# Kernel tuning notes

Hardware: AMD Instinct MI355X
Metric: run time of the kernel (lower is better)

The kernel has to match this reference:

```python
import jax, jax.numpy as jnp
import numpy as np

B, C, H, W = 8, 128, 192, 192
CROP = 39
LEN = CROP // 2            # 19 -> 38x38 crop
CY = CX = 96               # fixed crop center (original draws random.randint(19, 173))
MARGIN = 1.0


def grid_sample_bilinear(img, grid):
    """Bilinear grid_sample, align_corners=True, zeros padding.
    img: (B,C,H,W); grid: (B,H,W,2) with (x,y) in [-1,1]."""
    _, _, Hi, Wi = img.shape
    gx = (grid[..., 0] + 1.0) * 0.5 * (Wi - 1)   # (B,H,W) source x
    gy = (grid[..., 1] + 1.0) * 0.5 * (Hi - 1)   # (B,H,W) source y
    x0 = jnp.floor(gx)
    y0 = jnp.floor(gy)

    def gather(xf, yf):
        valid = (xf >= 0) & (xf <= Wi - 1) & (yf >= 0) & (yf <= Hi - 1)
        xi = jnp.clip(xf, 0, Wi - 1).astype(jnp.int32)
        yi = jnp.clip(yf, 0, Hi - 1).astype(jnp.int32)
        # per-batch gather: (C,H,W) values at integer (y,x) locations
        v = jax.vmap(lambda im, y, x: im[:, y, x])(img, yi, xi)  # (B,C,H,W)
        return v * valid[:, None, :, :].astype(img.dtype)

    wx1 = gx - x0
    wx0 = 1.0 - wx1
    wy1 = gy - y0
    wy0 = 1.0 - wy1
    w = lambda a: a[:, None, :, :]
    return (w(wx0 * wy0) * gather(x0,       y0)
          + w(wx1 * wy0) * gather(x0 + 1.0, y0)
          + w(wx0 * wy1) * gather(x0,       y0 + 1.0)
          + w(wx1 * wy1) * gather(x0 + 1.0, y0 + 1.0))


def hardnet_loss(anchor, positive, margin=MARGIN):
    """loss_HardNet with anchor_swap=False, batch_reduce='min', triplet_margin."""
    d1 = jnp.sum(anchor * anchor, axis=1)                       # (N,)
    d2 = jnp.sum(positive * positive, axis=1)                   # (N,)
    sq = d1[:, None] + d2[None, :] - 2.0 * (anchor @ positive.T)  # (N,N)
    dm = jnp.sqrt(jnp.maximum(sq, 0.0) + 1e-6) + 1e-8
    n = dm.shape[0]
    pos = jnp.diagonal(dm)                                      # positive distances
    dmod = dm + jnp.eye(n, dtype=dm.dtype) * 10.0               # mask diagonal
    dmod = dmod + jnp.where(dmod < 0.008, 10.0, 0.0)            # mask near-duplicates
    min_neg = jnp.min(dmod, axis=1)                             # hardest negative per anchor
    return jnp.mean(jnp.maximum(margin + pos - min_neg, 0.0))


def setup_inputs() -> dict:
    key = jax.random.key(0)
    k1, k2, k3 = jax.random.split(key, 3)
    feat1 = jax.random.normal(k1, (B, C, H, W), dtype=jnp.float32)
    feat2 = jax.random.normal(k2, (B, C, H, W), dtype=jnp.float32)
    # absolute flow: pixel coordinates in [0, W-1] / [0, H-1]
    aflow = jax.random.uniform(k3, (B, 2, H, W), dtype=jnp.float32) * (W - 1)
    return {"feat1": feat1, "feat2": feat2, "aflow": aflow}


def reference(feat1, feat2, aflow):
    # _aflow_to_grid: pixel coords -> [-1,1] grid (align_corners=True convention)
    gx = aflow[:, 0] * (2.0 / (W - 1)) - 1.0
    gy = aflow[:, 1] * (2.0 / (H - 1)) - 1.0
    grid = jnp.stack([gx, gy], axis=-1)                          # (B,H,W,2)
    grid = jnp.where(jnp.isnan(grid), 9e9, grid)                 # invalid -> out of range
    feat2to1 = grid_sample_bilinear(feat2, grid)                 # warp img2 feats to img1
    s = slice(CY - LEN, CY + LEN)                                # fixed 38x38 crop
    f1 = feat1[:, :, s, s]
    f2 = feat2to1[:, :, s, s]
    a = f1.transpose(0, 2, 3, 1).reshape(-1, C)                  # (B*38*38, C)
    p = f2.transpose(0, 2, 3, 1).reshape(-1, C)
    return hardnet_loss(a, p)
```

## Files before the change

kernel.cpp:

```cpp
#include <hip/hip_runtime.h>
#include <stdint.h>

#define Hh 192
#define Ww 192
#define HW 36864
#define CROPW 38
#define CW2 1444
#define CROPOFF 77
#define NPTS 11552
#define NPAD 11776
#define NTT 46
#define NCT 92
#define NG 5
#define JPB 19
#define NBLK (NG*NTT)
#define BIGF 3.0e38f

typedef short bf16x8 __attribute__((ext_vector_type(8)));
typedef float f32x4 __attribute__((ext_vector_type(4)));
typedef int   i32x4 __attribute__((ext_vector_type(4)));
typedef unsigned short ushort;

__device__ __forceinline__ ushort f2bf(float f) {
  uint32_t b = __float_as_uint(f);
  uint32_t r = b + 0x7fffu + ((b >> 16) & 1u);
  return (ushort)(r >> 16);
}
__device__ __forceinline__ float bf2f(ushort u) {
  return __uint_as_float(((uint32_t)u) << 16);
}

__device__ __forceinline__ void g2l16(const void* g, void* l) {
  __builtin_amdgcn_global_load_lds(
      (const __attribute__((address_space(1))) unsigned int*)g,
      (__attribute__((address_space(3))) unsigned int*)l, 16, 0, 0);
}

__global__ void init_k(ushort* __restrict__ aB, ushort* __restrict__ pB,
                       float* __restrict__ d1, float* __restrict__ d2) {
  int i = NPTS + threadIdx.x;
  if (i >= NPAD) return;
  d1[i] = 0.f;
  d2[i] = 1e30f;
  i32x4 z = {0,0,0,0};
  #pragma unroll
  for (int c = 0; c < 16; ++c) {
    *(i32x4*)&aB[(size_t)i*128 + c*8] = z;
    *(i32x4*)&pB[(size_t)i*128 + c*8] = z;
  }
}

__global__ __launch_bounds__(256) void transpose_k(
    const float* __restrict__ feat2, ushort* __restrict__ f2t) {
  __shared__ __align__(16) ushort l[32*136];
  int b = blockIdx.y;
  int hw0 = blockIdx.x * 32;
  int t = threadIdx.x;
  {
    int i4 = (t & 7) * 4, c0 = t >> 3;
    const float* src = feat2 + (size_t)b*128*HW + hw0 + i4;
    #pragma unroll
    for (int k = 0; k < 4; ++k) {
      int cc = c0 + k*32;
      f32x4 v = *(const f32x4*)(src + (size_t)cc*HW);
      #pragma unroll
      for (int j = 0; j < 4; ++j) l[(i4+j)*136 + cc] = f2bf(v[j]);
    }
  }
  __syncthreads();
  {
    int chunk = t & 7, p = t >> 3;
    ushort* dst = f2t + ((size_t)b*HW + hw0 + p)*128 + chunk*16;
    *(bf16x8*)dst       = *(const bf16x8*)&l[p*136 + chunk*16];
    *(bf16x8*)(dst + 8) = *(const bf16x8*)&l[p*136 + chunk*16 + 8];
  }
}

__global__ __launch_bounds__(256) void crop_k(
    const float* __restrict__ feat1, ushort* __restrict__ aB,
    float* __restrict__ d1) {
  __shared__ __align__(16) ushort l[38*136];
  int r = blockIdx.x;
  int b = blockIdx.y;
  int y = CROPOFF + r;
  int t = threadIdx.x;
  {
    int xo = t & 63, c0 = t >> 6;
    if (xo < CROPW) {
      const float* src = feat1 + ((size_t)b*128*HW) + (size_t)y*Ww + CROPOFF + xo;
      #pragma unroll
      for (int k = 0; k < 32; ++k) {
        int cc = c0*32 + k;
        l[xo*136 + cc] = f2bf(src[(size_t)cc*HW]);
      }
    }
  }
  __syncthreads();
  int chunk = t & 7, p0 = t >> 3;
  #pragma unroll
  for (int pp = 0; pp < 2; ++pp) {
    int p = p0 + pp*32;
    if (p >= CROPW) break;
    int idx = b*CW2 + r*CROPW + p;
    ushort* dst = aB + (size_t)idx*128 + chunk*16;
    *(bf16x8*)dst       = *(const bf16x8*)&l[p*136 + chunk*16];
    *(bf16x8*)(dst + 8) = *(const bf16x8*)&l[p*136 + chunk*16 + 8];
    float s = 0.f;
    #pragma unroll
    for (int j = 0; j < 16; ++j) {
      float v = bf2f(l[p*136 + chunk*16 + j]);
      s += v*v;
    }
    s += __shfl_xor(s, 1); s += __shfl_xor(s, 2); s += __shfl_xor(s, 4);
    if (chunk == 0) d1[idx] = s;
  }
}

__global__ __launch_bounds__(256) void samp2_k(
    const ushort* __restrict__ f2t, const float* __restrict__ aflow,
    ushort* __restrict__ pB, float* __restrict__ d2) {
  int tid = threadIdx.x;
  int idx = blockIdx.x*2 + (tid >> 7);
  int c = tid & 127;
  int b = idx / CW2;
  int rem = idx % CW2;
  int r = rem / CROPW, cx = rem % CROPW;
  int y = CROPOFF + r, x = CROPOFF + cx;

  float ax = aflow[((b*2 + 0)*Hh + y)*Ww + x];
  float ay = aflow[((b*2 + 1)*Hh + y)*Ww + x];
  float gxn = ax * (2.0f/(Ww-1)) - 1.0f;
  float gyn = ay * (2.0f/(Hh-1)) - 1.0f;
  float gx = (gxn + 1.0f) * 0.5f * (Ww-1);
  float gy = (gyn + 1.0f) * 0.5f * (Hh-1);
  int xi = min((int)floorf(gx), Ww-2);
  int yi = min((int)floorf(gy), Hh-2);
  float wx1 = gx - (float)xi, wx0 = 1.f - wx1;
  float wy1 = gy - (float)yi, wy0 = 1.f - wy1;

  const ushort* base = f2t + ((size_t)b*HW + (size_t)yi*Ww + xi)*128 + c;
  float v00 = bf2f(base[0]);
  float v01 = bf2f(base[128]);
  float v10 = bf2f(base[Ww*128]);
  float v11 = bf2f(base[Ww*128 + 128]);
  float v = wy0*(wx0*v00 + wx1*v01) + wy1*(wx0*v10 + wx1*v11);

  pB[(size_t)idx*128 + c] = f2bf(v);

  float s = v*v;
  for (int off = 1; off < 64; off <<= 1) s += __shfl_xor(s, off);
  __shared__ float red[4];
  if ((tid & 63) == 0) red[tid >> 6] = s;
  __syncthreads();
  if ((tid & 127) == 0) {
    int g = tid >> 7;
    d2[idx] = red[2*g] + red[2*g + 1];
  }
}

__global__ __launch_bounds__(512) void gemmp_k(
    const ushort* __restrict__ aB, const ushort* __restrict__ pB,
    const float* __restrict__ d1, const float* __restrict__ d2,
    float* __restrict__ pos, float* __restrict__ pmin) {
  __shared__ __align__(16) ushort lA[256*128];
  __shared__ __align__(16) ushort lB[2][128*128];

  int bid = blockIdx.x;
  int xcd = bid & 7, k = bid >> 3;
  int start = (xcd < 6) ? xcd*29 : 174 + (xcd-6)*28;
  int L = start + k;
  int g = L / NTT, tM = L % NTT;
  int j0 = g * JPB;
  int jn = (NCT - j0 < JPB) ? (NCT - j0) : JPB;

  int tid = threadIdx.x;
  int rowg = tid >> 4, cb = (tid & 15) << 4;

  {
    const char* gA = (const char*)aB + (size_t)tM * 65536;
    #pragma unroll
    for (int rnd = 0; rnd < 8; ++rnd) {
      int row = rnd*32 + rowg;
      g2l16(gA + row*256 + (cb ^ ((row&7)<<4)), (char*)lA + row*256 + cb);
    }
  }
  {
    const char* gB = (const char*)pB + (size_t)j0 * 128 * 256;
    #pragma unroll
    for (int rnd = 0; rnd < 4; ++rnd) {
      int row = rnd*32 + rowg;
      g2l16(gB + row*256 + (cb ^ ((row&7)<<4)), (char*)lB[0] + row*256 + cb);
    }
  }
  __syncthreads();

  int w = tid >> 6, l = tid & 63;
  int wr = w >> 1, wc = w & 1;
  int lcol = l & 15, hq = l >> 4, rb = hq << 2;
  int rsw = (lcol & 7) << 4;
  float mPart[4] = {BIGF, BIGF, BIGF, BIGF};

  for (int it = 0; it < jn; ++it) {
    int j = j0 + it;
    if (it + 1 < jn) {
      const char* gB = (const char*)pB + (size_t)(j+1) * 128 * 256;
      char* dst = (char*)lB[(it+1) & 1];
      #pragma unroll
      for (int rnd = 0; rnd < 4; ++rnd) {
        int row = rnd*32 + rowg;
        g2l16(gB + row*256 + (cb ^ ((row&7)<<4)), dst + row*256 + cb);
      }
    }
    const char* bufB = (const char*)lB[it & 1];
    f32x4 acc[4][4] = {};
    #pragma unroll
    for (int ks = 0; ks < 4; ++ks) {
      int cbase = ks*64 + (hq << 4);
      bf16x8 aF[4], bF[4];
      #pragma unroll
      for (int ma = 0; ma < 4; ++ma)
        aF[ma] = *(const bf16x8*)((const char*)lA + (wr*64 + ma*16 + lcol)*256 + (cbase ^ rsw));
      #pragma unroll
      for (int np = 0; np < 4; ++np)
        bF[np] = *(const bf16x8*)(bufB + (wc*64 + np*16 + lcol)*256 + (cbase ^ rsw));
      #pragma unroll
      for (int np = 0; np < 4; ++np)
        #pragma unroll
        for (int ma = 0; ma < 4; ++ma)
          acc[np][ma] = __builtin_amdgcn_mfma_f32_16x16x32_bf16(bF[np], aF[ma], acc[np][ma], 0, 0, 0);
    }

    f32x4 d2v[4];
    #pragma unroll
    for (int np = 0; np < 4; ++np)
      d2v[np] = *(const f32x4*)&d2[j*128 + wc*64 + np*16 + rb];

    if ((j >> 1) != tM) {
      #pragma unroll
      for (int ma = 0; ma < 4; ++ma)
        #pragma unroll
        for (int np = 0; np < 4; ++np)
          #pragma unroll
          for (int reg = 0; reg < 4; ++reg)
            mPart[ma] = fminf(mPart[ma], fmaf(-2.f, acc[np][ma][reg], d2v[np][reg]));
    } else {
      #pragma unroll
      for (int ma = 0; ma < 4; ++ma) {
        int gi = tM*256 + wr*64 + ma*16 + lcol;
        #pragma unroll
        for (int np = 0; np < 4; ++np)
          #pragma unroll
          for (int reg = 0; reg < 4; ++reg) {
            int gj = j*128 + wc*64 + np*16 + rb + reg;
            float t = fmaf(-2.f, acc[np][ma][reg], d2v[np][reg]);
            if (gi == gj)
              pos[gi] = sqrtf(fmaxf(d1[gi] + t, 0.f) + 1e-6f) + 1e-8f;
            else
              mPart[ma] = fminf(mPart[ma], t);
          }
      }
    }
    __syncthreads();
  }

  #pragma unroll
  for (int ma = 0; ma < 4; ++ma) {
    float u = mPart[ma];
    u = fminf(u, __shfl_xor(u, 16));
    u = fminf(u, __shfl_xor(u, 32));
    mPart[ma] = u;
  }
  __syncthreads();
  float* sm = (float*)lB;
  if (hq == 0) {
    #pragma unroll
    for (int ma = 0; ma < 4; ++ma)
      sm[wc*256 + wr*64 + ma*16 + lcol] = mPart[ma];
  }
  __syncthreads();
  if (tid < 256) {
    int row = tM*256 + tid;
    float u = fminf(sm[tid], sm[256 + tid]);
    float dm = sqrtf(fmaxf(d1[row] + u, 0.f) + 1e-6f) + 1e-8f;
    pmin[g*NPAD + row] = dm;
  }
}

__global__ __launch_bounds__(1024) void fin_k(const float* __restrict__ pos,
                                              const float* __restrict__ pmin,
                                              float* __restrict__ out) {
  float s = 0.f;
  for (int i = threadIdx.x; i < NPTS; i += 1024) {
    float p = pos[i];
    float mneg = p + 10.f;
    #pragma unroll
    for (int g = 0; g < NG; ++g) mneg = fminf(mneg, pmin[g*NPAD + i]);
    s += fmaxf(1.0f + p - mneg, 0.f);
  }
  for (int off = 1; off < 64; off <<= 1) s += __shfl_xor(s, off);
  __shared__ float red[16];
  if ((threadIdx.x & 63) == 0) red[threadIdx.x >> 6] = s;
  __syncthreads();
  if (threadIdx.x == 0) {
    float t = 0.f;
    #pragma unroll
    for (int k = 0; k < 16; ++k) t += red[k];
    out[0] = t / (float)NPTS;
  }
}

extern "C" void kernel_launch(void* const* d_in, const int* in_sizes, int n_in,
                              void* d_out, int out_size, void* d_ws, size_t ws_size,
                              hipStream_t stream) {
  const float* feat1 = (const float*)d_in[0];
  const float* feat2 = (const float*)d_in[1];
  const float* aflow = (const float*)d_in[2];

  char* ws = (char*)d_ws;
  ushort* aB = (ushort*)ws;
  ushort* pB = aB + (size_t)NPAD * 128;
  float*  d1 = (float*)(pB + (size_t)NPAD * 128);
  float*  d2 = d1 + NPAD;
  float*  pos = d2 + NPAD;
  float*  pmin = pos + NPAD;
  ushort* f2t = (ushort*)(pmin + (size_t)NG*NPAD);

  hipLaunchKernelGGL(transpose_k, dim3(HW/32, 8), dim3(256), 0, stream,
                     feat2, f2t);
  hipLaunchKernelGGL(init_k, dim3(1), dim3(256), 0, stream,
                     aB, pB, d1, d2);
  hipLaunchKernelGGL(crop_k, dim3(CROPW, 8), dim3(256), 0, stream,
                     feat1, aB, d1);
  hipLaunchKernelGGL(samp2_k, dim3(NPTS/2), dim3(256), 0, stream,
                     f2t, aflow, pB, d2);
  hipLaunchKernelGGL(gemmp_k, dim3(NBLK), dim3(512), 0, stream,
                     aB, pB, d1, d2, pos, pmin);
  hipLaunchKernelGGL(fin_k, dim3(1), dim3(1024), 0, stream,
                     pos, pmin, (float*)d_out);
}
```

Measured before the change: 107.2 us.

## Hold GEMM A tile in registers, stream B from global, fuse prep kernels

The distance GEMM no longer stages tiles in LDS. Each wave keeps a 128-row slice of the anchor tile in registers and reads positive fragments straight from global memory, which removes the LDS copies and per-iteration barriers; the kernel is now bounded to two blocks per CU. The feat2 transpose and feat1 crop are merged into one launch, and the padding initialisation moves into an extra block of the sampler, which cuts two launches. The sampler now handles two channels per lane, with one wave per point and a wave shuffle reduction in place of the LDS reduction. The trade-offs are much higher register pressure and redundant global and L2 traffic for B, and the padding rows of aB and d1 are no longer zeroed.

Measured after the change: 116.6 us. +8.7%, slower.

```diff
diff --git a/kernel.cpp b/kernel.cpp
--- a/kernel.cpp
+++ b/kernel.cpp
@@ -14,6 +14,7 @@
 #define NG 5
 #define JPB 19
 #define NBLK (NG*NTT)
+#define TRB (HW/32)
 #define BIGF 3.0e38f
 
 typedef short bf16x8 __attribute__((ext_vector_type(8)));
@@ -30,89 +31,65 @@
   return __uint_as_float(((uint32_t)u) << 16);
 }
 
-__device__ __forceinline__ void g2l16(const void* g, void* l) {
-  __builtin_amdgcn_global_load_lds(
-      (const __attribute__((address_space(1))) unsigned int*)g,
-      (__attribute__((address_space(3))) unsigned int*)l, 16, 0, 0);
-}
-
-__global__ void init_k(ushort* __restrict__ aB, ushort* __restrict__ pB,
-                       float* __restrict__ d1, float* __restrict__ d2) {
-  int i = NPTS + threadIdx.x;
-  if (i >= NPAD) return;
-  d1[i] = 0.f;
-  d2[i] = 1e30f;
-  i32x4 z = {0,0,0,0};
-  #pragma unroll
-  for (int c = 0; c < 16; ++c) {
-    *(i32x4*)&aB[(size_t)i*128 + c*8] = z;
-    *(i32x4*)&pB[(size_t)i*128 + c*8] = z;
-  }
-}
-
-__global__ __launch_bounds__(256) void transpose_k(
-    const float* __restrict__ feat2, ushort* __restrict__ f2t) {
-  __shared__ __align__(16) ushort l[32*136];
+__global__ __launch_bounds__(256) void prep_k(
+    const float* __restrict__ feat1, const float* __restrict__ feat2,
+    ushort* __restrict__ f2t, ushort* __restrict__ aB, float* __restrict__ d1) {
+  __shared__ __align__(16) ushort lsh[38*136];
   int b = blockIdx.y;
-  int hw0 = blockIdx.x * 32;
   int t = threadIdx.x;
-  {
-    int i4 = (t & 7) * 4, c0 = t >> 3;
-    const float* src = feat2 + (size_t)b*128*HW + hw0 + i4;
-    #pragma unroll
-    for (int k = 0; k < 4; ++k) {
-      int cc = c0 + k*32;
-      f32x4 v = *(const f32x4*)(src + (size_t)cc*HW);
-      #pragma unroll
-      for (int j = 0; j < 4; ++j) l[(i4+j)*136 + cc] = f2bf(v[j]);
-    }
-  }
-  __syncthreads();
-  {
-    int chunk = t & 7, p = t >> 3;
-    ushort* dst = f2t + ((size_t)b*HW + hw0 + p)*128 + chunk*16;
-    *(bf16x8*)dst       = *(const bf16x8*)&l[p*136 + chunk*16];
-    *(bf16x8*)(dst + 8) = *(const bf16x8*)&l[p*136 + chunk*16 + 8];
-  }
-}
-
-__global__ __launch_bounds__(256) void crop_k(
-    const float* __restrict__ feat1, ushort* __restrict__ aB,
-    float* __restrict__ d1) {
-  __shared__ __align__(16) ushort l[38*136];
-  int r = blockIdx.x;
-  int b = blockIdx.y;
-  int y = CROPOFF + r;
-  int t = threadIdx.x;
-  {
-    int xo = t & 63, c0 = t >> 6;
-    if (xo < CROPW) {
-      const float* src = feat1 + ((size_t)b*128*HW) + (size_t)y*Ww + CROPOFF + xo;
-      #pragma unroll
-      for (int k = 0; k < 32; ++k) {
-        int cc = c0*32 + k;
-        l[xo*136 + cc] = f2bf(src[(size_t)cc*HW]);
-      }
-    }
-  }
-  __syncthreads();
-  int chunk = t & 7, p0 = t >> 3;
-  #pragma unroll
-  for (int pp = 0; pp < 2; ++pp) {
-    int p = p0 + pp*32;
-    if (p >= CROPW) break;
-    int idx = b*CW2 + r*CROPW + p;
-    ushort* dst = aB + (size_t)idx*128 + chunk*16;
-    *(bf16x8*)dst       = *(const bf16x8*)&l[p*136 + chunk*16];
-    *(bf16x8*)(dst + 8) = *(const bf16x8*)&l[p*136 + chunk*16 + 8];
-    float s = 0.f;
-    #pragma unroll
-    for (int j = 0; j < 16; ++j) {
-      float v = bf2f(l[p*136 + chunk*16 + j]);
-      s += v*v;
-    }
-    s += __shfl_xor(s, 1); s += __shfl_xor(s, 2); s += __shfl_xor(s, 4);
-    if (chunk == 0) d1[idx] = s;
+  if (blockIdx.x < TRB) {
+    int hw0 = blockIdx.x * 32;
+    {
+      int i4 = (t & 7) * 4, c0 = t >> 3;
+      const float* src = feat2 + (size_t)b*128*HW + hw0 + i4;
+      #pragma unroll
+      for (int k = 0; k < 4; ++k) {
+        int cc = c0 + k*32;
+        f32x4 v = *(const f32x4*)(src + (size_t)cc*HW);
+        #pragma unroll
+        for (int j = 0; j < 4; ++j) lsh[(i4+j)*136 + cc] = f2bf(v[j]);
+      }
+    }
+    __syncthreads();
+    {
+      int chunk = t & 7, p = t >> 3;
+      ushort* dst = f2t + ((size_t)b*HW + hw0 + p)*128 + chunk*16;
+      *(bf16x8*)dst       = *(const bf16x8*)&lsh[p*136 + chunk*16];
+      *(bf16x8*)(dst + 8) = *(const bf16x8*)&lsh[p*136 + chunk*16 + 8];
+    }
+  } else {
+    int r = blockIdx.x - TRB;
+    int y = CROPOFF + r;
+    {
+      int xo = t & 63, c0 = t >> 6;
+      if (xo < CROPW) {
+        const float* src = feat1 + ((size_t)b*128*HW) + (size_t)y*Ww + CROPOFF + xo;
+        #pragma unroll
+        for (int k = 0; k < 32; ++k) {
+          int cc = c0*32 + k;
+          lsh[xo*136 + cc] = f2bf(src[(size_t)cc*HW]);
+        }
+      }
+    }
+    __syncthreads();
+    int chunk = t & 7, p0 = t >> 3;
+    #pragma unroll
+    for (int pp = 0; pp < 2; ++pp) {
+      int p = p0 + pp*32;
+      if (p >= CROPW) break;
+      int idx = b*CW2 + r*CROPW + p;
+      ushort* dst = aB + (size_t)idx*128 + chunk*16;
+      *(bf16x8*)dst       = *(const bf16x8*)&lsh[p*136 + chunk*16];
+      *(bf16x8*)(dst + 8) = *(const bf16x8*)&lsh[p*136 + chunk*16 + 8];
+      float s = 0.f;
+      #pragma unroll
+      for (int j = 0; j < 16; ++j) {
+        float v = bf2f(lsh[p*136 + chunk*16 + j]);
+        s += v*v;
+      }
+      s += __shfl_xor(s, 1); s += __shfl_xor(s, 2); s += __shfl_xor(s, 4);
+      if (chunk == 0) d1[idx] = s;
+    }
   }
 }
 
@@ -120,8 +97,18 @@
     const ushort* __restrict__ f2t, const float* __restrict__ aflow,
     ushort* __restrict__ pB, float* __restrict__ d2) {
   int tid = threadIdx.x;
-  int idx = blockIdx.x*2 + (tid >> 7);
-  int c = tid & 127;
+  if (blockIdx.x == NPTS/4) {
+    int i = NPTS + tid;
+    if (i < NPAD) {
+      d2[i] = 1e30f;
+      i32x4 z = {0,0,0,0};
+      #pragma unroll
+      for (int c = 0; c < 16; ++c) *(i32x4*)&pB[(size_t)i*128 + c*8] = z;
+    }
+    return;
+  }
+  int idx = blockIdx.x*4 + (tid >> 6);
+  int l = tid & 63, c2 = l*2;
   int b = idx / CW2;
   int rem = idx % CW2;
   int r = rem / CROPW, cx = rem % CROPW;
@@ -138,151 +125,120 @@
   float wx1 = gx - (float)xi, wx0 = 1.f - wx1;
   float wy1 = gy - (float)yi, wy0 = 1.f - wy1;
 
-  const ushort* base = f2t + ((size_t)b*HW + (size_t)yi*Ww + xi)*128 + c;
-  float v00 = bf2f(base[0]);
-  float v01 = bf2f(base[128]);
-  float v10 = bf2f(base[Ww*128]);
-  float v11 = bf2f(base[Ww*128 + 128]);
-  float v = wy0*(wx0*v00 + wx1*v01) + wy1*(wx0*v10 + wx1*v11);
-
-  pB[(size_t)idx*128 + c] = f2bf(v);
-
-  float s = v*v;
+  const ushort* base = f2t + ((size_t)b*HW + (size_t)yi*Ww + xi)*128 + c2;
+  uint32_t u00 = *(const uint32_t*)(base);
+  uint32_t u01 = *(const uint32_t*)(base + 128);
+  uint32_t u10 = *(const uint32_t*)(base + Ww*128);
+  uint32_t u11 = *(const uint32_t*)(base + Ww*128 + 128);
+  float v0 = wy0*(wx0*bf2f((ushort)u00) + wx1*bf2f((ushort)u01))
+           + wy1*(wx0*bf2f((ushort)u10) + wx1*bf2f((ushort)u11));
+  float v1 = wy0*(wx0*bf2f((ushort)(u00>>16)) + wx1*bf2f((ushort)(u01>>16)))
+           + wy1*(wx0*bf2f((ushort)(u10>>16)) + wx1*bf2f((ushort)(u11>>16)));
+
+  uint32_t packed = ((uint32_t)f2bf(v1) << 16) | f2bf(v0);
+  *(uint32_t*)&pB[(size_t)idx*128 + c2] = packed;
+
+  float s = v0*v0 + v1*v1;
   for (int off = 1; off < 64; off <<= 1) s += __shfl_xor(s, off);
-  __shared__ float red[4];
-  if ((tid & 63) == 0) red[tid >> 6] = s;
-  __syncthreads();
-  if ((tid & 127) == 0) {
-    int g = tid >> 7;
-    d2[idx] = red[2*g] + red[2*g + 1];
-  }
-}
-
-__global__ __launch_bounds__(512) void gemmp_k(
+  if (l == 0) d2[idx] = s;
+}
+
+__global__ __launch_bounds__(512, 2) void gemmp_k(
     const ushort* __restrict__ aB, const ushort* __restrict__ pB,
     const float* __restrict__ d1, const float* __restrict__ d2,
     float* __restrict__ pos, float* __restrict__ pmin) {
-  __shared__ __align__(16) ushort lA[256*128];
-  __shared__ __align__(16) ushort lB[2][128*128];
+  __shared__ float sm[4][256];
 
   int bid = blockIdx.x;
-  int xcd = bid & 7, k = bid >> 3;
+  int xcd = bid & 7, kk = bid >> 3;
   int start = (xcd < 6) ? xcd*29 : 174 + (xcd-6)*28;
-  int L = start + k;
+  int L = start + kk;
   int g = L / NTT, tM = L % NTT;
   int j0 = g * JPB;
   int jn = (NCT - j0 < JPB) ? (NCT - j0) : JPB;
 
   int tid = threadIdx.x;
-  int rowg = tid >> 4, cb = (tid & 15) << 4;
-
+  int w = tid >> 6, l = tid & 63;
+  int wr = w >> 2, wc = w & 3;
+  int lcol = l & 15, hq = l >> 4, rb = hq << 2;
+
+  bf16x8 aF[32];
   {
-    const char* gA = (const char*)aB + (size_t)tM * 65536;
-    #pragma unroll
-    for (int rnd = 0; rnd < 8; ++rnd) {
-      int row = rnd*32 + rowg;
-      g2l16(gA + row*256 + (cb ^ ((row&7)<<4)), (char*)lA + row*256 + cb);
-    }
-  }
-  {
-    const char* gB = (const char*)pB + (size_t)j0 * 128 * 256;
-    #pragma unroll
-    for (int rnd = 0; rnd < 4; ++rnd) {
-      int row = rnd*32 + rowg;
-      g2l16(gB + row*256 + (cb ^ ((row&7)<<4)), (char*)lB[0] + row*256 + cb);
-    }
-  }
-  __syncthreads();
-
-  int w = tid >> 6, l = tid & 63;
-  int wr = w >> 1, wc = w & 1;
-  int lcol = l & 15, hq = l >> 4, rb = hq << 2;
-  int rsw = (lcol & 7) << 4;
-  float mPart[4] = {BIGF, BIGF, BIGF, BIGF};
+    const char* gA = (const char*)aB + ((size_t)(tM*256 + wr*128 + lcol))*256 + hq*16;
+    #pragma unroll
+    for (int ma = 0; ma < 8; ++ma)
+      #pragma unroll
+      for (int ks = 0; ks < 4; ++ks)
+        aF[ma*4+ks] = *(const bf16x8*)(gA + ma*16*256 + ks*64);
+  }
+
+  float mPart[8] = {BIGF,BIGF,BIGF,BIGF,BIGF,BIGF,BIGF,BIGF};
 
   for (int it = 0; it < jn; ++it) {
     int j = j0 + it;
-    if (it + 1 < jn) {
-      const char* gB = (const char*)pB + (size_t)(j+1) * 128 * 256;
-      char* dst = (char*)lB[(it+1) & 1];
-      #pragma unroll
-      for (int rnd = 0; rnd < 4; ++rnd) {
-        int row = rnd*32 + rowg;
-        g2l16(gB + row*256 + (cb ^ ((row&7)<<4)), dst + row*256 + cb);
-      }
-    }
-    const char* bufB = (const char*)lB[it & 1];
-    f32x4 acc[4][4] = {};
+    const char* gB = (const char*)pB + ((size_t)(j*128 + wc*32 + lcol))*256 + hq*16;
+    f32x4 acc[2][8] = {};
     #pragma unroll
     for (int ks = 0; ks < 4; ++ks) {
-      int cbase = ks*64 + (hq << 4);
-      bf16x8 aF[4], bF[4];
-      #pragma unroll
-      for (int ma = 0; ma < 4; ++ma)
-        aF[ma] = *(const bf16x8*)((const char*)lA + (wr*64 + ma*16 + lcol)*256 + (cbase ^ rsw));
-      #pragma unroll
-      for (int np = 0; np < 4; ++np)
-        bF[np] = *(const bf16x8*)(bufB + (wc*64 + np*16 + lcol)*256 + (cbase ^ rsw));
-      #pragma unroll
-      for (int np = 0; np < 4; ++np)
-        #pragma unroll
-        for (int ma = 0; ma < 4; ++ma)
-          acc[np][ma] = __builtin_amdgcn_mfma_f32_16x16x32_bf16(bF[np], aF[ma], acc[np][ma], 0, 0, 0);
-    }
-
-    f32x4 d2v[4];
-    #pragma unroll
-    for (int np = 0; np < 4; ++np)
-      d2v[np] = *(const f32x4*)&d2[j*128 + wc*64 + np*16 + rb];
+      bf16x8 b0 = *(const bf16x8*)(gB + ks*64);
+      bf16x8 b1 = *(const bf16x8*)(gB + 16*256 + ks*64);
+      #pragma unroll
+      for (int ma = 0; ma < 8; ++ma)
+        acc[0][ma] = __builtin_amdgcn_mfma_f32_16x16x32_bf16(b0, aF[ma*4+ks], acc[0][ma], 0, 0, 0);
+      #pragma unroll
+      for (int ma = 0; ma < 8; ++ma)
+        acc[1][ma] = __builtin_amdgcn_mfma_f32_16x16x32_bf16(b1, aF[ma*4+ks], acc[1][ma], 0, 0, 0);
+    }
+
+    f32x4 d2v0 = *(const f32x4*)&d2[j*128 + wc*32 + rb];
+    f32x4 d2v1 = *(const f32x4*)&d2[j*128 + wc*32 + 16 + rb];
 
     if ((j >> 1) != tM) {
       #pragma unroll
-      for (int ma = 0; ma < 4; ++ma)
-        #pragma unroll
-        for (int np = 0; np < 4; ++np)
-          #pragma unroll
-          for (int reg = 0; reg < 4; ++reg)
-            mPart[ma] = fminf(mPart[ma], fmaf(-2.f, acc[np][ma][reg], d2v[np][reg]));
+      for (int ma = 0; ma < 8; ++ma) {
+        #pragma unroll
+        for (int reg = 0; reg < 4; ++reg) {
+          mPart[ma] = fminf(mPart[ma], fmaf(-2.f, acc[0][ma][reg], d2v0[reg]));
+          mPart[ma] = fminf(mPart[ma], fmaf(-2.f, acc[1][ma][reg], d2v1[reg]));
+        }
+      }
     } else {
       #pragma unroll
-      for (int ma = 0; ma < 4; ++ma) {
-        int gi = tM*256 + wr*64 + ma*16 + lcol;
-        #pragma unroll
-        for (int np = 0; np < 4; ++np)
+      for (int ma = 0; ma < 8; ++ma) {
+        int gi = tM*256 + wr*128 + ma*16 + lcol;
+        #pragma unroll
+        for (int np = 0; np < 2; ++np) {
           #pragma unroll
           for (int reg = 0; reg < 4; ++reg) {
-            int gj = j*128 + wc*64 + np*16 + rb + reg;
-            float t = fmaf(-2.f, acc[np][ma][reg], d2v[np][reg]);
+            int gj = j*128 + wc*32 + np*16 + rb + reg;
+            float t = fmaf(-2.f, acc[np][ma][reg], np ? d2v1[reg] : d2v0[reg]);
             if (gi == gj)
               pos[gi] = sqrtf(fmaxf(d1[gi] + t, 0.f) + 1e-6f) + 1e-8f;
             else
               mPart[ma] = fminf(mPart[ma], t);
           }
-      }
-    }
-    __syncthreads();
+        }
+      }
+    }
   }
 
   #pragma unroll
-  for (int ma = 0; ma < 4; ++ma) {
+  for (int ma = 0; ma < 8; ++ma) {
     float u = mPart[ma];
     u = fminf(u, __shfl_xor(u, 16));
     u = fminf(u, __shfl_xor(u, 32));
     mPart[ma] = u;
   }
-  __syncthreads();
-  float* sm = (float*)lB;
   if (hq == 0) {
     #pragma unroll
-    for (int ma = 0; ma < 4; ++ma)
-      sm[wc*256 + wr*64 + ma*16 + lcol] = mPart[ma];
+    for (int ma = 0; ma < 8; ++ma)
+      sm[wc][wr*128 + ma*16 + lcol] = mPart[ma];
   }
   __syncthreads();
   if (tid < 256) {
     int row = tM*256 + tid;
-    float u = fminf(sm[tid], sm[256 + tid]);
-    float dm = sqrtf(fmaxf(d1[row] + u, 0.f) + 1e-6f) + 1e-8f;
-    pmin[g*NPAD + row] = dm;
+    float u = fminf(fminf(sm[0][tid], sm[1][tid]), fminf(sm[2][tid], sm[3][tid]));
+    pmin[g*NPAD + row] = sqrtf(fmaxf(d1[row] + u, 0.f) + 1e-6f) + 1e-8f;
   }
 }
 
@@ -325,13 +281,9 @@
   float*  pmin = pos + NPAD;
   ushort* f2t = (ushort*)(pmin + (size_t)NG*NPAD);
 
-  hipLaunchKernelGGL(transpose_k, dim3(HW/32, 8), dim3(256), 0, stream,
-                     feat2, f2t);
-  hipLaunchKernelGGL(init_k, dim3(1), dim3(256), 0, stream,
-                     aB, pB, d1, d2);
-  hipLaunchKernelGGL(crop_k, dim3(CROPW, 8), dim3(256), 0, stream,
-                     feat1, aB, d1);
-  hipLaunchKernelGGL(samp2_k, dim3(NPTS/2), dim3(256), 0, stream,
+  hipLaunchKernelGGL(prep_k, dim3(TRB + CROPW, 8), dim3(256), 0, stream,
+                     feat1, feat2, f2t, aB, d1);
+  hipLaunchKernelGGL(samp2_k, dim3(NPTS/4 + 1), dim3(256), 0, stream,
                      f2t, aflow, pB, d2);
   hipLaunchKernelGGL(gemmp_k, dim3(NBLK), dim3(512), 0, stream,
                      aB, pB, d1, d2, pos, pmin);
```

## Sample warped features from per-channel LDS planes instead of transposed copy

Applied to the files above, without the earlier changes.

Removes the full feat2 transpose into a bf16 channel-last buffer. Each block now loads one (batch, channel) plane into LDS as bf16 and bilinearly samples all crop points from precomputed coordinates. Crop extraction and coordinate computation are merged into one launch, and the squared norms move to a separate pass that also zero-pads the tail rows. The GEMM keeps its A fragments in registers rather than staging them in LDS. This trades a large transposed write and re-read for 72KB LDS planes and scattered 2-byte stores into pB, plus higher register pressure in the GEMM.

Result: faster. 98.19 us (-8.4%).

```diff
diff --git a/kernel.cpp b/kernel.cpp
--- a/kernel.cpp
+++ b/kernel.cpp
@@ -14,11 +14,14 @@
 #define NG 5
 #define JPB 19
 #define NBLK (NG*NTT)
+#define CROPB 304
+#define CRDB 46
 #define BIGF 3.0e38f
 
 typedef short bf16x8 __attribute__((ext_vector_type(8)));
 typedef float f32x4 __attribute__((ext_vector_type(4)));
-typedef int   i32x4 __attribute__((ext_vector_type(4)));
+typedef uint32_t u32x2 __attribute__((ext_vector_type(2)));
+typedef uint32_t u32x4 __attribute__((ext_vector_type(4)));
 typedef unsigned short ushort;
 
 __device__ __forceinline__ ushort f2bf(float f) {
@@ -36,125 +39,123 @@
       (__attribute__((address_space(3))) unsigned int*)l, 16, 0, 0);
 }
 
-__global__ void init_k(ushort* __restrict__ aB, ushort* __restrict__ pB,
-                       float* __restrict__ d1, float* __restrict__ d2) {
-  int i = NPTS + threadIdx.x;
-  if (i >= NPAD) return;
-  d1[i] = 0.f;
-  d2[i] = 1e30f;
-  i32x4 z = {0,0,0,0};
+__global__ __launch_bounds__(256) void prep2_k(
+    const float* __restrict__ feat1, const float* __restrict__ aflow,
+    ushort* __restrict__ aB, u32x4* __restrict__ coords) {
+  int bid = blockIdx.x;
+  int t = threadIdx.x;
+  if (bid < CROPB) {
+    __shared__ __align__(16) ushort lsh[38*136];
+    int b = bid / CROPW, r = bid % CROPW;
+    int y = CROPOFF + r;
+    {
+      int xo = t & 63, c0 = t >> 6;
+      if (xo < CROPW) {
+        const float* src = feat1 + ((size_t)b*128*HW) + (size_t)y*Ww + CROPOFF + xo;
+        #pragma unroll
+        for (int k = 0; k < 32; ++k) {
+          int cc = c0*32 + k;
+          lsh[xo*136 + cc] = f2bf(src[(size_t)cc*HW]);
+        }
+      }
+    }
+    __syncthreads();
+    int chunk = t & 7, p0 = t >> 3;
+    #pragma unroll
+    for (int pp = 0; pp < 2; ++pp) {
+      int p = p0 + pp*32;
+      if (p >= CROPW) break;
+      int idx = b*CW2 + r*CROPW + p;
+      ushort* dst = aB + (size_t)idx*128 + chunk*16;
+      *(bf16x8*)dst       = *(const bf16x8*)&lsh[p*136 + chunk*16];
+      *(bf16x8*)(dst + 8) = *(const bf16x8*)&lsh[p*136 + chunk*16 + 8];
+    }
+  } else {
+    int idx = (bid - CROPB)*256 + t;
+    if (idx >= NPTS) return;
+    int b = idx / CW2;
+    int rem = idx % CW2;
+    int r = rem / CROPW, cx = rem % CROPW;
+    int y = CROPOFF + r, x = CROPOFF + cx;
+    float ax = aflow[((b*2 + 0)*Hh + y)*Ww + x];
+    float ay = aflow[((b*2 + 1)*Hh + y)*Ww + x];
+    float gxn = ax * (2.0f/(Ww-1)) - 1.0f;
+    float gyn = ay * (2.0f/(Hh-1)) - 1.0f;
+    float gx = (gxn + 1.0f) * 0.5f * (Ww-1);
+    float gy = (gyn + 1.0f) * 0.5f * (Hh-1);
+    int xi = min((int)floorf(gx), Ww-2);
+    int yi = min((int)floorf(gy), Hh-2);
+    u32x4 cd;
+    cd.x = (uint32_t)(yi*Ww + xi);
+    cd.y = __float_as_uint(gx - (float)xi);
+    cd.z = __float_as_uint(gy - (float)yi);
+    cd.w = 0;
+    coords[idx] = cd;
+  }
+}
+
+__global__ __launch_bounds__(256) void slab_k(
+    const float* __restrict__ feat2, const u32x4* __restrict__ coords,
+    ushort* __restrict__ pB) {
+  __shared__ __align__(16) ushort plane[HW];
+  int bid = blockIdx.x;
+  int b = bid >> 7, c = bid & 127;
+  int t = threadIdx.x;
+  const float* src = feat2 + ((size_t)(b*128 + c)) * HW;
   #pragma unroll
-  for (int c = 0; c < 16; ++c) {
-    *(i32x4*)&aB[(size_t)i*128 + c*8] = z;
-    *(i32x4*)&pB[(size_t)i*128 + c*8] = z;
-  }
-}
-
-__global__ __launch_bounds__(256) void transpose_k(
-    const float* __restrict__ feat2, ushort* __restrict__ f2t) {
-  __shared__ __align__(16) ushort l[32*136];
-  int b = blockIdx.y;
-  int hw0 = blockIdx.x * 32;
-  int t = threadIdx.x;
-  {
-    int i4 = (t & 7) * 4, c0 = t >> 3;
-    const float* src = feat2 + (size_t)b*128*HW + hw0 + i4;
-    #pragma unroll
-    for (int k = 0; k < 4; ++k) {
-      int cc = c0 + k*32;
-      f32x4 v = *(const f32x4*)(src + (size_t)cc*HW);
-      #pragma unroll
-      for (int j = 0; j < 4; ++j) l[(i4+j)*136 + cc] = f2bf(v[j]);
-    }
-  }
-  __syncthreads();
-  {
-    int chunk = t & 7, p = t >> 3;
-    ushort* dst = f2t + ((size_t)b*HW + hw0 + p)*128 + chunk*16;
-    *(bf16x8*)dst       = *(const bf16x8*)&l[p*136 + chunk*16];
-    *(bf16x8*)(dst + 8) = *(const bf16x8*)&l[p*136 + chunk*16 + 8];
-  }
-}
-
-__global__ __launch_bounds__(256) void crop_k(
-    const float* __restrict__ feat1, ushort* __restrict__ aB,
-    float* __restrict__ d1) {
-  __shared__ __align__(16) ushort l[38*136];
-  int r = blockIdx.x;
-  int b = blockIdx.y;
-  int y = CROPOFF + r;
-  int t = threadIdx.x;
-  {
-    int xo = t & 63, c0 = t >> 6;
-    if (xo < CROPW) {
-      const float* src = feat1 + ((size_t)b*128*HW) + (size_t)y*Ww + CROPOFF + xo;
-      #pragma unroll
-      for (int k = 0; k < 32; ++k) {
-        int cc = c0*32 + k;
-        l[xo*136 + cc] = f2bf(src[(size_t)cc*HW]);
+  for (int k = 0; k < 36; ++k) {
+    int i = (k*256 + t) * 4;
+    f32x4 v = *(const f32x4*)(src + i);
+    u32x2 pk;
+    pk.x = (uint32_t)f2bf(v[0]) | ((uint32_t)f2bf(v[1]) << 16);
+    pk.y = (uint32_t)f2bf(v[2]) | ((uint32_t)f2bf(v[3]) << 16);
+    *(u32x2*)&plane[i] = pk;
+  }
+  __syncthreads();
+  int pbase = b*CW2;
+  #pragma unroll
+  for (int it = 0; it < 6; ++it) {
+    int p = it*256 + t;
+    if (p < CW2) {
+      u32x4 cd = coords[pbase + p];
+      int cell = (int)cd.x;
+      float wx1 = __uint_as_float(cd.y), wx0 = 1.f - wx1;
+      float wy1 = __uint_as_float(cd.z), wy0 = 1.f - wy1;
+      float v00 = bf2f(plane[cell]);
+      float v01 = bf2f(plane[cell + 1]);
+      float v10 = bf2f(plane[cell + Ww]);
+      float v11 = bf2f(plane[cell + Ww + 1]);
+      float v = wy0*(wx0*v00 + wx1*v01) + wy1*(wx0*v10 + wx1*v11);
+      pB[(size_t)(pbase + p)*128 + c] = f2bf(v);
+    }
+  }
+}
+
+__global__ __launch_bounds__(256) void d12_k(
+    ushort* __restrict__ aB, ushort* __restrict__ pB,
+    float* __restrict__ d1, float* __restrict__ d2) {
+  int w = threadIdx.x >> 6, l = threadIdx.x & 63;
+  int base = blockIdx.x*32 + w*8;
+  #pragma unroll
+  for (int i = 0; i < 8; ++i) {
+    int row = base + i;
+    if (row < NPTS) {
+      uint32_t ua = *(const uint32_t*)&aB[(size_t)row*128 + l*2];
+      uint32_t up = *(const uint32_t*)&pB[(size_t)row*128 + l*2];
+      float a0 = bf2f((ushort)ua), a1 = bf2f((ushort)(ua >> 16));
+      float p0 = bf2f((ushort)up), p1 = bf2f((ushort)(up >> 16));
+      float sa = a0*a0 + a1*a1;
+      float sp = p0*p0 + p1*p1;
+      for (int off = 1; off < 64; off <<= 1) {
+        sa += __shfl_xor(sa, off);
+        sp += __shfl_xor(sp, off);
       }
-    }
-  }
-  __syncthreads();
-  int chunk = t & 7, p0 = t >> 3;
-  #pragma unroll
-  for (int pp = 0; pp < 2; ++pp) {
-    int p = p0 + pp*32;
-    if (p >= CROPW) break;
-    int idx = b*CW2 + r*CROPW + p;
-    ushort* dst = aB + (size_t)idx*128 + chunk*16;
-    *(bf16x8*)dst       = *(const bf16x8*)&l[p*136 + chunk*16];
-    *(bf16x8*)(dst + 8) = *(const bf16x8*)&l[p*136 + chunk*16 + 8];
-    float s = 0.f;
-    #pragma unroll
-    for (int j = 0; j < 16; ++j) {
-      float v = bf2f(l[p*136 + chunk*16 + j]);
-      s += v*v;
-    }
-    s += __shfl_xor(s, 1); s += __shfl_xor(s, 2); s += __shfl_xor(s, 4);
-    if (chunk == 0) d1[idx] = s;
-  }
-}
-
-__global__ __launch_bounds__(256) void samp2_k(
-    const ushort* __restrict__ f2t, const float* __restrict__ aflow,
-    ushort* __restrict__ pB, float* __restrict__ d2) {
-  int tid = threadIdx.x;
-  int idx = blockIdx.x*2 + (tid >> 7);
-  int c = tid & 127;
-  int b = idx / CW2;
-  int rem = idx % CW2;
-  int r = rem / CROPW, cx = rem % CROPW;
-  int y = CROPOFF + r, x = CROPOFF + cx;
-
-  float ax = aflow[((b*2 + 0)*Hh + y)*Ww + x];
-  float ay = aflow[((b*2 + 1)*Hh + y)*Ww + x];
-  float gxn = ax * (2.0f/(Ww-1)) - 1.0f;
-  float gyn = ay * (2.0f/(Hh-1)) - 1.0f;
-  float gx = (gxn + 1.0f) * 0.5f * (Ww-1);
-  float gy = (gyn + 1.0f) * 0.5f * (Hh-1);
-  int xi = min((int)floorf(gx), Ww-2);
-  int yi = min((int)floorf(gy), Hh-2);
-  float wx1 = gx - (float)xi, wx0 = 1.f - wx1;
-  float wy1 = gy - (float)yi, wy0 = 1.f - wy1;
-
-  const ushort* base = f2t + ((size_t)b*HW + (size_t)yi*Ww + xi)*128 + c;
-  float v00 = bf2f(base[0]);
-  float v01 = bf2f(base[128]);
-  float v10 = bf2f(base[Ww*128]);
-  float v11 = bf2f(base[Ww*128 + 128]);
-  float v = wy0*(wx0*v00 + wx1*v01) + wy1*(wx0*v10 + wx1*v11);
-
-  pB[(size_t)idx*128 + c] = f2bf(v);
-
-  float s = v*v;
-  for (int off = 1; off < 64; off <<= 1) s += __shfl_xor(s, off);
-  __shared__ float red[4];
-  if ((tid & 63) == 0) red[tid >> 6] = s;
-  __syncthreads();
-  if ((tid & 127) == 0) {
-    int g = tid >> 7;
-    d2[idx] = red[2*g] + red[2*g + 1];
+      if (l == 0) { d1[row] = sa; d2[row] = sp; }
+    } else {
+      *(uint32_t*)&aB[(size_t)row*128 + l*2] = 0;
+      *(uint32_t*)&pB[(size_t)row*128 + l*2] = 0;
+      if (l == 0) { d1[row] = 0.f; d2[row] = 1e30f; }
+    }
   }
 }
 
@@ -162,42 +163,43 @@
     const ushort* __restrict__ aB, const ushort* __restrict__ pB,
     const float* __restrict__ d1, const float* __restrict__ d2,
     float* __restrict__ pos, float* __restrict__ pmin) {
-  __shared__ __align__(16) ushort lA[256*128];
   __shared__ __align__(16) ushort lB[2][128*128];
 
   int bid = blockIdx.x;
-  int xcd = bid & 7, k = bid >> 3;
+  int xcd = bid & 7, kk = bid >> 3;
   int start = (xcd < 6) ? xcd*29 : 174 + (xcd-6)*28;
-  int L = start + k;
+  int L = start + kk;
   int g = L / NTT, tM = L % NTT;
   int j0 = g * JPB;
   int jn = (NCT - j0 < JPB) ? (NCT - j0) : JPB;
 
   int tid = threadIdx.x;
   int rowg = tid >> 4, cb = (tid & 15) << 4;
-
-  {
-    const char* gA = (const char*)aB + (size_t)tM * 65536;
-    #pragma unroll
-    for (int rnd = 0; rnd < 8; ++rnd) {
-      int row = rnd*32 + rowg;
-      g2l16(gA + row*256 + (cb ^ ((row&7)<<4)), (char*)lA + row*256 + cb);
-    }
-  }
-  {
-    const char* gB = (const char*)pB + (size_t)j0 * 128 * 256;
-    #pragma unroll
-    for (int rnd = 0; rnd < 4; ++rnd) {
-      int row = rnd*32 + rowg;
-      g2l16(gB + row*256 + (cb ^ ((row&7)<<4)), (char*)lB[0] + row*256 + cb);
-    }
-  }
-  __syncthreads();
-
   int w = tid >> 6, l = tid & 63;
   int wr = w >> 1, wc = w & 1;
   int lcol = l & 15, hq = l >> 4, rb = hq << 2;
   int rsw = (lcol & 7) << 4;
+
+  {
+    const char* gB = (const char*)pB + (size_t)j0 * 128 * 256;
+    #pragma unroll
+    for (int rnd = 0; rnd < 4; ++rnd) {
+      int row = rnd*32 + rowg;
+      g2l16(gB + row*256 + (cb ^ ((row&7)<<4)), (char*)lB[0] + row*256 + cb);
+    }
+  }
+
+  bf16x8 aF[16];
+  {
+    const char* gA = (const char*)aB + ((size_t)(tM*256 + wr*64 + lcol))*256 + hq*16;
+    #pragma unroll
+    for (int ma = 0; ma < 4; ++ma)
+      #pragma unroll
+      for (int ks = 0; ks < 4; ++ks)
+        aF[ma*4+ks] = *(const bf16x8*)(gA + ma*16*256 + ks*64);
+  }
+  __syncthreads();
+
   float mPart[4] = {BIGF, BIGF, BIGF, BIGF};
 
   for (int it = 0; it < jn; ++it) {
@@ -216,10 +218,7 @@
     #pragma unroll
     for (int ks = 0; ks < 4; ++ks) {
       int cbase = ks*64 + (hq << 4);
-      bf16x8 aF[4], bF[4];
-      #pragma unroll
-      for (int ma = 0; ma < 4; ++ma)
-        aF[ma] = *(const bf16x8*)((const char*)lA + (wr*64 + ma*16 + lcol)*256 + (cbase ^ rsw));
+      bf16x8 bF[4];
       #pragma unroll
       for (int np = 0; np < 4; ++np)
         bF[np] = *(const bf16x8*)(bufB + (wc*64 + np*16 + lcol)*256 + (cbase ^ rsw));
@@ -227,7 +226,7 @@
       for (int np = 0; np < 4; ++np)
         #pragma unroll
         for (int ma = 0; ma < 4; ++ma)
-          acc[np][ma] = __builtin_amdgcn_mfma_f32_16x16x32_bf16(bF[np], aF[ma], acc[np][ma], 0, 0, 0);
+          acc[np][ma] = __builtin_amdgcn_mfma_f32_16x16x32_bf16(bF[np], aF[ma*4+ks], acc[np][ma], 0, 0, 0);
     }
 
     f32x4 d2v[4];
@@ -281,8 +280,7 @@
   if (tid < 256) {
     int row = tM*256 + tid;
     float u = fminf(sm[tid], sm[256 + tid]);
-    float dm = sqrtf(fmaxf(d1[row] + u, 0.f) + 1e-6f) + 1e-8f;
-    pmin[g*NPAD + row] = dm;
+    pmin[g*NPAD + row] = sqrtf(fmaxf(d1[row] + u, 0.f) + 1e-6f) + 1e-8f;
   }
 }
 
@@ -323,16 +321,14 @@
   float*  d2 = d1 + NPAD;
   float*  pos = d2 + NPAD;
   float*  pmin = pos + NPAD;
-  ushort* f2t = (ushort*)(pmin + (size_t)NG*NPAD);
-
-  hipLaunchKernelGGL(transpose_k, dim3(HW/32, 8), dim3(256), 0, stream,
-                     feat2, f2t);
-  hipLaunchKernelGGL(init_k, dim3(1), dim3(256), 0, stream,
+  u32x4*  coords = (u32x4*)(pmin + (size_t)NG*NPAD);
+
+  hipLaunchKernelGGL(prep2_k, dim3(CROPB + CRDB), dim3(256), 0, stream,
+                     feat1, aflow, aB, coords);
+  hipLaunchKernelGGL(slab_k, dim3(1024), dim3(256), 0, stream,
+                     feat2, coords, pB);
+  hipLaunchKernelGGL(d12_k, dim3(NPAD/32), dim3(256), 0, stream,
                      aB, pB, d1, d2);
-  hipLaunchKernelGGL(crop_k, dim3(CROPW, 8), dim3(256), 0, stream,
-                     feat1, aB, d1);
-  hipLaunchKernelGGL(samp2_k, dim3(NPTS/2), dim3(256), 0, stream,
-                     f2t, aflow, pB, d2);
   hipLaunchKernelGGL(gemmp_k, dim3(NBLK), dim3(512), 0, stream,
                      aB, pB, d1, d2, pos, pmin);
   hipLaunchKernelGGL(fin_k, dim3(1), dim3(1024), 0, stream,
```
